# Performance work log

Hardware: AMD Instinct MI355X
Metric: run time of the kernel (lower is better)

Reference implementation:

```python
import jax, jax.numpy as jnp
import numpy as np

INPUT_SIZE = 16
HIDDEN = 256


def setup_inputs() -> dict:
    key = jax.random.key(0)
    ks = jax.random.split(key, 12)
    B, T, F, H = 512, 168, INPUT_SIZE, HIDDEN
    s_ih = 1.0 / np.sqrt(H)
    def u(k, shape):
        return jax.random.uniform(k, shape, jnp.float32, -s_ih, s_ih)
    return {
        "x": jax.random.normal(ks[0], (B, T, F), jnp.float32),
        # LSTM params, torch gate order (i, f, g, o) stacked along dim 0
        "w_ih": u(ks[1], (4 * H, F)),
        "w_hh": u(ks[2], (4 * H, H)),
        "b_ih": u(ks[3], (4 * H,)),
        "b_hh": u(ks[4], (4 * H,)),
        # MLP params
        "fc1_w": u(ks[5], (128, H)),
        "fc1_b": u(ks[6], (128,)),
        "fc2_w": u(ks[7], (64, 128)),
        "fc2_b": u(ks[8], (64,)),
        "fc3_w": u(ks[9], (1, 64)),
        "fc3_b": u(ks[10], (1,)),
    }


def _lstm(x, w_ih, w_hh, b_ih, b_hh):
    B, T, F = x.shape
    H = w_hh.shape[1]
    # Precompute input contribution for all timesteps: [B, T, 4H]
    x_proj = jnp.einsum("btf,gf->btg", x, w_ih) + b_ih + b_hh

    def step(carry, xp_t):
        h, c = carry
        gates = xp_t + h @ w_hh.T  # [B, 4H]
        i, f, g, o = jnp.split(gates, 4, axis=-1)
        i = jax.nn.sigmoid(i)
        f = jax.nn.sigmoid(f)
        g = jnp.tanh(g)
        o = jax.nn.sigmoid(o)
        c = f * c + i * g
        h = o * jnp.tanh(c)
        return (h, c), h

    h0 = jnp.zeros((B, H), x.dtype)
    c0 = jnp.zeros((B, H), x.dtype)
    (_, _), hs = jax.lax.scan(step, (h0, c0), jnp.swapaxes(x_proj, 0, 1))
    return jnp.swapaxes(hs, 0, 1)  # [B, T, H]


def reference(x, w_ih, w_hh, b_ih, b_hh, fc1_w, fc1_b, fc2_w, fc2_b, fc3_w, fc3_b):
    h = _lstm(x, w_ih, w_hh, b_ih, b_hh)          # [B, T, H]
    h = jax.nn.relu(h @ fc1_w.T + fc1_b)           # [B, T, 128]
    h = jax.nn.relu(h @ fc2_w.T + fc2_b)           # [B, T, 64]
    out = h @ fc3_w.T + fc3_b                      # [B, T, 1]
    return out
```

## Files before the change

### kernel.cpp

```cpp
#include <hip/hip_runtime.h>

typedef _Float16 half8 __attribute__((ext_vector_type(8)));
typedef float floatx4 __attribute__((ext_vector_type(4)));
typedef unsigned uint4v __attribute__((ext_vector_type(4)));

#define Bsz 512
#define Tsz 168
#define Fsz 16
#define Hsz 256
#define KTILES 9
#define LDS_K 296

#define WSW_OFF   0
#define BIAS_OFF  589824
#define FC1_OFF   593920
#define FC2_OFF   659456
#define HH_OFF    675840
#define XBUF_OFF  (HH_OFF + 44040192)

__global__ __launch_bounds__(256) void k_prep(
    const float* __restrict__ w_hh, const float* __restrict__ w_ih,
    const float* __restrict__ b_ih, const float* __restrict__ b_hh,
    const float* __restrict__ fc1_w, const float* __restrict__ fc2_w,
    _Float16* __restrict__ wsw, float* __restrict__ bias,
    _Float16* __restrict__ w1f, _Float16* __restrict__ w2f) {
    const int b = blockIdx.x, tid = threadIdx.x;
    const int lane = tid & 63, sub = tid >> 6;
    if (b < 144) {
        int tile = b * 4 + sub;
        int nt = tile / KTILES, kt = tile - nt * KTILES;
        int n_in = lane & 15, kg = lane >> 4;
        int J = nt >> 2, g = nt & 3;
        int n_orig = g * 256 + J * 16 + n_in;
        half8 v;
#pragma unroll
        for (int e = 0; e < 8; ++e) {
            int k = kt * 32 + kg * 8 + e;
            float f;
            if (k < 256)      f = w_hh[n_orig * 256 + k];
            else if (k < 272) f = w_ih[n_orig * 16 + (k - 256)];
            else              f = 0.0f;
            v[e] = (_Float16)f;
        }
        ((half8*)wsw)[tile * 64 + lane] = v;
    } else if (b < 148) {
        int id = (b - 144) * 256 + tid;
        int nt = id >> 4, n = id & 15;
        int J = nt >> 2, g = nt & 3;
        int n_orig = g * 256 + J * 16 + n;
        bias[id] = b_ih[n_orig] + b_hh[n_orig];
    } else if (b < 164) {
        int tile = (b - 148) * 4 + sub;
        int nt = tile >> 3, kt = tile & 7;
        int n_in = lane & 15, kg = lane >> 4;
        half8 v;
#pragma unroll
        for (int e = 0; e < 8; ++e)
            v[e] = (_Float16)fc1_w[(nt * 16 + n_in) * 256 + kt * 32 + kg * 8 + e];
        ((half8*)w1f)[tile * 64 + lane] = v;
    } else {
        int tile = (b - 164) * 4 + sub;
        int nt = tile >> 2, kt = tile & 3;
        int n_in = lane & 15, kg = lane >> 4;
        half8 v;
#pragma unroll
        for (int e = 0; e < 8; ++e)
            v[e] = (_Float16)fc2_w[(nt * 16 + n_in) * 128 + kt * 32 + kg * 8 + e];
        ((half8*)w2f)[tile * 64 + lane] = v;
    }
}

__global__ __launch_bounds__(512, 1) void k_lstm14(
    const float* __restrict__ x, const _Float16* __restrict__ wsw,
    const float* __restrict__ bias, unsigned* __restrict__ hh32,
    unsigned long long* __restrict__ xbuf) {
    __shared__ __align__(16) _Float16 h_lds[16][LDS_K];
    __shared__ float glds[4][16][68];

    const int tid = threadIdx.x;
    const int wave = tid >> 6, lane = tid & 63;
    const int n_in = lane & 15, quad = lane >> 4;
    const int bb = blockIdx.x & 31, ng = blockIdx.x >> 5;
    const int b0 = bb * 16;
    const int Jl = wave & 3;
    const int gp = wave >> 2;

    float bs[2];
    half8 wf[2][KTILES];
#pragma unroll
    for (int gg = 0; gg < 2; ++gg) {
        const int nt = ng * 16 + Jl * 4 + gp * 2 + gg;
        bs[gg] = bias[nt * 16 + n_in];
#pragma unroll
        for (int kt = 0; kt < KTILES; ++kt)
            wf[gg][kt] = ((const half8*)wsw)[((size_t)nt * KTILES + kt) * 64 + lane];
    }

    for (int i = tid; i < 16 * LDS_K; i += 512)
        ((_Float16*)h_lds)[i] = (_Float16)0.0f;
    __syncthreads();
    if (tid < 256) {
        int m = tid >> 4, f = tid & 15;
        h_lds[m][Hsz + f] = (_Float16)x[((b0 + m) * Tsz + 0) * Fsz + f];
    }
    __syncthreads();

    const int cm = tid >> 5, cj = tid & 31;
    float c_st[2] = {0.f, 0.f};

    for (int t = 0; t < Tsz; ++t) {
        half8 afr[KTILES];
#pragma unroll
        for (int kt = 0; kt < KTILES; ++kt)
            afr[kt] = *(const half8*)&h_lds[n_in][kt * 32 + quad * 8];

        floatx4 acc[2] = {(floatx4){0.f,0.f,0.f,0.f}, (floatx4){0.f,0.f,0.f,0.f}};
#pragma unroll
        for (int gg = 0; gg < 2; ++gg) {
#pragma unroll
            for (int kt = 0; kt < KTILES; ++kt)
                acc[gg] = __builtin_amdgcn_mfma_f32_16x16x32_f16(afr[kt], wf[gg][kt], acc[gg], 0, 0, 0);
        }

#pragma unroll
        for (int gg = 0; gg < 2; ++gg)
#pragma unroll
            for (int r = 0; r < 4; ++r)
                glds[gp * 2 + gg][quad * 4 + r][Jl * 16 + n_in] = acc[gg][r] + bs[gg];
        __syncthreads();

        union { _Float16 f[2]; unsigned u; } pk;
#pragma unroll
        for (int e = 0; e < 2; ++e) {
            int jl = 2 * cj + e;
            float ig = glds[0][cm][jl];
            float fg = glds[1][cm][jl];
            float gg_ = glds[2][cm][jl];
            float og = glds[3][cm][jl];
            float si = 1.0f / (1.0f + __expf(-ig));
            float sf = 1.0f / (1.0f + __expf(-fg));
            float tg = 1.0f - 2.0f / (__expf(2.0f * gg_) + 1.0f);
            float so = 1.0f / (1.0f + __expf(-og));
            float c = sf * c_st[e] + si * tg;
            c_st[e] = c;
            float th = 1.0f - 2.0f / (__expf(2.0f * c) + 1.0f);
            pk.f[e] = (_Float16)(so * th);
        }
        *(unsigned*)&h_lds[cm][ng * 64 + 2 * cj] = pk.u;

        const size_t rb = ((size_t)((bb * 2 + (t & 1)) * 16));
        if (t + 1 < Tsz) {
            unsigned long long pv = ((unsigned long long)pk.u << 32) | (unsigned)(t + 1);
            __hip_atomic_store(&xbuf[(rb + cm) * 128 + ng * 32 + cj], pv,
                               __ATOMIC_RELAXED, __HIP_MEMORY_SCOPE_AGENT);
        }
        __builtin_nontemporal_store(
            pk.u, &hh32[((size_t)(b0 + cm) * Tsz + t) * 128 + ng * 32 + cj]);

        if (t + 1 < Tsz) {
            float xr = 0.0f;
            if (tid < 256)
                xr = x[((b0 + (tid >> 4)) * Tsz + (t + 1)) * Fsz + (tid & 15)];

            const unsigned want = (unsigned)(t + 1);
            unsigned long long* p1 = &xbuf[(rb + cm) * 128 + ((ng + 1) & 3) * 32 + cj];
            unsigned long long* p2 = &xbuf[(rb + cm) * 128 + ((ng + 2) & 3) * 32 + cj];
            unsigned long long* p3 = &xbuf[(rb + cm) * 128 + ((ng + 3) & 3) * 32 + cj];
            unsigned long long v1 = __hip_atomic_load(p1, __ATOMIC_RELAXED,
                                                      __HIP_MEMORY_SCOPE_AGENT);
            unsigned long long v2 = __hip_atomic_load(p2, __ATOMIC_RELAXED,
                                                      __HIP_MEMORY_SCOPE_AGENT);
            unsigned long long v3 = __hip_atomic_load(p3, __ATOMIC_RELAXED,
                                                      __HIP_MEMORY_SCOPE_AGENT);
            while ((unsigned)v1 != want || (unsigned)v2 != want || (unsigned)v3 != want) {
                if ((unsigned)v1 != want)
                    v1 = __hip_atomic_load(p1, __ATOMIC_RELAXED, __HIP_MEMORY_SCOPE_AGENT);
                if ((unsigned)v2 != want)
                    v2 = __hip_atomic_load(p2, __ATOMIC_RELAXED, __HIP_MEMORY_SCOPE_AGENT);
                if ((unsigned)v3 != want)
                    v3 = __hip_atomic_load(p3, __ATOMIC_RELAXED, __HIP_MEMORY_SCOPE_AGENT);
            }
            *(unsigned*)&h_lds[cm][((ng + 1) & 3) * 64 + 2 * cj] = (unsigned)(v1 >> 32);
            *(unsigned*)&h_lds[cm][((ng + 2) & 3) * 64 + 2 * cj] = (unsigned)(v2 >> 32);
            *(unsigned*)&h_lds[cm][((ng + 3) & 3) * 64 + 2 * cj] = (unsigned)(v3 >> 32);
            if (tid < 256)
                h_lds[tid >> 4][Hsz + (tid & 15)] = (_Float16)xr;
            __syncthreads();
        }
    }
}

__global__ __launch_bounds__(512, 1) void k_mlp5(
    const _Float16* __restrict__ hh, const _Float16* __restrict__ w1f,
    const _Float16* __restrict__ w2f, const float* __restrict__ b1,
    const float* __restrict__ b2, const float* __restrict__ w3,
    const float* __restrict__ b3, float* __restrict__ out) {
    __shared__ __align__(16) _Float16 w1sh[64 * 512];
    __shared__ __align__(16) _Float16 w2sh[16 * 512];
    __shared__ _Float16 st1[8][16][136];
    __shared__ _Float16 st2[8][16][72];

    const int tid = threadIdx.x;
    const int wave = tid >> 6, lane = tid & 63;
    const int n_in = lane & 15, quad = lane >> 4;
    const int nchunks = (Bsz * Tsz) / 128;

    {
        float4* d1 = (float4*)w1sh;
        const float4* s1 = (const float4*)w1f;
#pragma unroll
        for (int it = 0; it < 8; ++it) d1[it * 512 + tid] = s1[it * 512 + tid];
        float4* d2 = (float4*)w2sh;
        const float4* s2 = (const float4*)w2f;
#pragma unroll
        for (int it = 0; it < 2; ++it) d2[it * 512 + tid] = s2[it * 512 + tid];
    }
    __syncthreads();

    uint4v rawA[8], rawB[8];
    if (blockIdx.x < nchunks) {
        const int tok0 = blockIdx.x * 128 + wave * 16;
#pragma unroll
        for (int kt = 0; kt < 8; ++kt)
            rawA[kt] = __builtin_nontemporal_load(
                (const uint4v*)&hh[(size_t)(tok0 + n_in) * 256 + kt * 32 + quad * 8]);
    }

    for (int chunk = blockIdx.x; chunk < nchunks; chunk += gridDim.x) {
        const int nxt = chunk + gridDim.x;
        if (nxt < nchunks) {
            const int tok0n = nxt * 128 + wave * 16;
#pragma unroll
            for (int kt = 0; kt < 8; ++kt)
                rawB[kt] = __builtin_nontemporal_load(
                    (const uint4v*)&hh[(size_t)(tok0n + n_in) * 256 + kt * 32 + quad * 8]);
        }

        const int tok0 = chunk * 128 + wave * 16;
        half8 afr[8];
#pragma unroll
        for (int kt = 0; kt < 8; ++kt)
            afr[kt] = __builtin_bit_cast(half8, rawA[kt]);

#pragma unroll
        for (int nt = 0; nt < 8; ++nt) {
            floatx4 a = (floatx4){0.f, 0.f, 0.f, 0.f};
#pragma unroll
            for (int kt = 0; kt < 8; ++kt) {
                half8 bfr = *(const half8*)&w1sh[(nt * 8 + kt) * 512 + lane * 8];
                a = __builtin_amdgcn_mfma_f32_16x16x32_f16(afr[kt], bfr, a, 0, 0, 0);
            }
            float bb = b1[nt * 16 + n_in];
#pragma unroll
            for (int r = 0; r < 4; ++r) {
                float v = a[r] + bb;
                st1[wave][quad * 4 + r][nt * 16 + n_in] = (_Float16)(v > 0.f ? v : 0.f);
            }
        }

        half8 a2[4];
#pragma unroll
        for (int kt = 0; kt < 4; ++kt)
            a2[kt] = *(const half8*)&st1[wave][n_in][kt * 32 + quad * 8];
#pragma unroll
        for (int nt = 0; nt < 4; ++nt) {
            floatx4 a = (floatx4){0.f, 0.f, 0.f, 0.f};
#pragma unroll
            for (int kt = 0; kt < 4; ++kt) {
                half8 bfr = *(const half8*)&w2sh[(nt * 4 + kt) * 512 + lane * 8];
                a = __builtin_amdgcn_mfma_f32_16x16x32_f16(a2[kt], bfr, a, 0, 0, 0);
            }
            float bb = b2[nt * 16 + n_in];
#pragma unroll
            for (int r = 0; r < 4; ++r) {
                float v = a[r] + bb;
                st2[wave][quad * 4 + r][nt * 16 + n_in] = (_Float16)(v > 0.f ? v : 0.f);
            }
        }

        float p = 0.0f;
#pragma unroll
        for (int e = 0; e < 16; ++e)
            p += (float)st2[wave][n_in][quad * 16 + e] * w3[quad * 16 + e];
        p += __shfl_down(p, 32);
        p += __shfl_down(p, 16);
        if (quad == 0) out[tok0 + n_in] = p + b3[0];

#pragma unroll
        for (int kt = 0; kt < 8; ++kt) rawA[kt] = rawB[kt];
    }
}

extern "C" void kernel_launch(void* const* d_in, const int* in_sizes, int n_in,
                              void* d_out, int out_size, void* d_ws, size_t ws_size,
                              hipStream_t stream) {
    const float* x     = (const float*)d_in[0];
    const float* w_ih  = (const float*)d_in[1];
    const float* w_hh  = (const float*)d_in[2];
    const float* b_ih  = (const float*)d_in[3];
    const float* b_hh  = (const float*)d_in[4];
    const float* fc1_w = (const float*)d_in[5];
    const float* fc1_b = (const float*)d_in[6];
    const float* fc2_w = (const float*)d_in[7];
    const float* fc2_b = (const float*)d_in[8];
    const float* fc3_w = (const float*)d_in[9];
    const float* fc3_b = (const float*)d_in[10];

    char* ws = (char*)d_ws;
    _Float16* wsw  = (_Float16*)(ws + WSW_OFF);
    float*    bias = (float*)(ws + BIAS_OFF);
    _Float16* w1f  = (_Float16*)(ws + FC1_OFF);
    _Float16* w2f  = (_Float16*)(ws + FC2_OFF);
    _Float16* hhist= (_Float16*)(ws + HH_OFF);
    unsigned long long* xbuf = (unsigned long long*)(ws + XBUF_OFF);

    k_prep<<<168, 256, 0, stream>>>(w_hh, w_ih, b_ih, b_hh, fc1_w, fc2_w,
                                    wsw, bias, w1f, w2f);
    k_lstm14<<<128, 512, 0, stream>>>(x, wsw, bias, (unsigned*)hhist, xbuf);
    k_mlp5<<<224, 512, 0, stream>>>(hhist, w1f, w2f, fc1_b, fc2_b,
                                    fc3_w, fc3_b, (float*)d_out);
}
```

Measured before the change: 423.3 us.

## Drop prep kernel, convert weights in-kernel, fixed 3-chunk MLP prefetch

Removes the separate weight-prep kernel; the LSTM and MLP kernels now read fp32 weights and convert them to fp16 fragments themselves, which saves one launch and a workspace round trip. The x load for the next step is moved to the start of each timestep, the local h store is moved after the atomic publish, and the spin loop reloads all three flags unconditionally. The MLP kernel replaces its strided double-buffered loop with three chunk loads issued up front and then computed, which assumes exactly 672 chunks across 224 blocks. Launch bounds change to allow 2 blocks per CU, which may raise register pressure.

```diff
diff --git a/kernel.cpp b/kernel.cpp
--- a/kernel.cpp
+++ b/kernel.cpp
@@ -11,68 +11,13 @@
 #define KTILES 9
 #define LDS_K 296
 
-#define WSW_OFF   0
-#define BIAS_OFF  589824
-#define FC1_OFF   593920
-#define FC2_OFF   659456
 #define HH_OFF    675840
 #define XBUF_OFF  (HH_OFF + 44040192)
 
-__global__ __launch_bounds__(256) void k_prep(
-    const float* __restrict__ w_hh, const float* __restrict__ w_ih,
-    const float* __restrict__ b_ih, const float* __restrict__ b_hh,
-    const float* __restrict__ fc1_w, const float* __restrict__ fc2_w,
-    _Float16* __restrict__ wsw, float* __restrict__ bias,
-    _Float16* __restrict__ w1f, _Float16* __restrict__ w2f) {
-    const int b = blockIdx.x, tid = threadIdx.x;
-    const int lane = tid & 63, sub = tid >> 6;
-    if (b < 144) {
-        int tile = b * 4 + sub;
-        int nt = tile / KTILES, kt = tile - nt * KTILES;
-        int n_in = lane & 15, kg = lane >> 4;
-        int J = nt >> 2, g = nt & 3;
-        int n_orig = g * 256 + J * 16 + n_in;
-        half8 v;
-#pragma unroll
-        for (int e = 0; e < 8; ++e) {
-            int k = kt * 32 + kg * 8 + e;
-            float f;
-            if (k < 256)      f = w_hh[n_orig * 256 + k];
-            else if (k < 272) f = w_ih[n_orig * 16 + (k - 256)];
-            else              f = 0.0f;
-            v[e] = (_Float16)f;
-        }
-        ((half8*)wsw)[tile * 64 + lane] = v;
-    } else if (b < 148) {
-        int id = (b - 144) * 256 + tid;
-        int nt = id >> 4, n = id & 15;
-        int J = nt >> 2, g = nt & 3;
-        int n_orig = g * 256 + J * 16 + n;
-        bias[id] = b_ih[n_orig] + b_hh[n_orig];
-    } else if (b < 164) {
-        int tile = (b - 148) * 4 + sub;
-        int nt = tile >> 3, kt = tile & 7;
-        int n_in = lane & 15, kg = lane >> 4;
-        half8 v;
-#pragma unroll
-        for (int e = 0; e < 8; ++e)
-            v[e] = (_Float16)fc1_w[(nt * 16 + n_in) * 256 + kt * 32 + kg * 8 + e];
-        ((half8*)w1f)[tile * 64 + lane] = v;
-    } else {
-        int tile = (b - 164) * 4 + sub;
-        int nt = tile >> 2, kt = tile & 3;
-        int n_in = lane & 15, kg = lane >> 4;
-        half8 v;
-#pragma unroll
-        for (int e = 0; e < 8; ++e)
-            v[e] = (_Float16)fc2_w[(nt * 16 + n_in) * 128 + kt * 32 + kg * 8 + e];
-        ((half8*)w2f)[tile * 64 + lane] = v;
-    }
-}
-
-__global__ __launch_bounds__(512, 1) void k_lstm14(
-    const float* __restrict__ x, const _Float16* __restrict__ wsw,
-    const float* __restrict__ bias, unsigned* __restrict__ hh32,
+__global__ __launch_bounds__(512, 2) void k_lstm15(
+    const float* __restrict__ x, const float* __restrict__ w_ih,
+    const float* __restrict__ w_hh, const float* __restrict__ b_ih,
+    const float* __restrict__ b_hh, unsigned* __restrict__ hh32,
     unsigned long long* __restrict__ xbuf) {
     __shared__ __align__(16) _Float16 h_lds[16][LDS_K];
     __shared__ float glds[4][16][68];
@@ -84,16 +29,34 @@
     const int b0 = bb * 16;
     const int Jl = wave & 3;
     const int gp = wave >> 2;
+    (void)wave;
 
     float bs[2];
     half8 wf[2][KTILES];
 #pragma unroll
     for (int gg = 0; gg < 2; ++gg) {
         const int nt = ng * 16 + Jl * 4 + gp * 2 + gg;
-        bs[gg] = bias[nt * 16 + n_in];
-#pragma unroll
-        for (int kt = 0; kt < KTILES; ++kt)
-            wf[gg][kt] = ((const half8*)wsw)[((size_t)nt * KTILES + kt) * 64 + lane];
+        const int J = nt >> 2, g = nt & 3;
+        const int n_orig = g * 256 + J * 16 + n_in;
+        bs[gg] = b_ih[n_orig] + b_hh[n_orig];
+#pragma unroll
+        for (int kt = 0; kt < 8; ++kt) {
+            const float* src = &w_hh[n_orig * 256 + kt * 32 + quad * 8];
+            half8 v;
+#pragma unroll
+            for (int e = 0; e < 8; ++e) v[e] = (_Float16)src[e];
+            wf[gg][kt] = v;
+        }
+        half8 vx;
+        if (quad < 2) {
+            const float* srcx = &w_ih[n_orig * 16 + quad * 8];
+#pragma unroll
+            for (int e = 0; e < 8; ++e) vx[e] = (_Float16)srcx[e];
+        } else {
+#pragma unroll
+            for (int e = 0; e < 8; ++e) vx[e] = (_Float16)0.0f;
+        }
+        wf[gg][8] = vx;
     }
 
     for (int i = tid; i < 16 * LDS_K; i += 512)
@@ -109,6 +72,10 @@
     float c_st[2] = {0.f, 0.f};
 
     for (int t = 0; t < Tsz; ++t) {
+        float xr = 0.0f;
+        if (t + 1 < Tsz && tid < 256)
+            xr = x[((b0 + (tid >> 4)) * Tsz + (t + 1)) * Fsz + (tid & 15)];
+
         half8 afr[KTILES];
 #pragma unroll
         for (int kt = 0; kt < KTILES; ++kt)
@@ -146,7 +113,6 @@
             float th = 1.0f - 2.0f / (__expf(2.0f * c) + 1.0f);
             pk.f[e] = (_Float16)(so * th);
         }
-        *(unsigned*)&h_lds[cm][ng * 64 + 2 * cj] = pk.u;
 
         const size_t rb = ((size_t)((bb * 2 + (t & 1)) * 16));
         if (t + 1 < Tsz) {
@@ -154,14 +120,11 @@
             __hip_atomic_store(&xbuf[(rb + cm) * 128 + ng * 32 + cj], pv,
                                __ATOMIC_RELAXED, __HIP_MEMORY_SCOPE_AGENT);
         }
+        *(unsigned*)&h_lds[cm][ng * 64 + 2 * cj] = pk.u;
         __builtin_nontemporal_store(
             pk.u, &hh32[((size_t)(b0 + cm) * Tsz + t) * 128 + ng * 32 + cj]);
 
         if (t + 1 < Tsz) {
-            float xr = 0.0f;
-            if (tid < 256)
-                xr = x[((b0 + (tid >> 4)) * Tsz + (t + 1)) * Fsz + (tid & 15)];
-
             const unsigned want = (unsigned)(t + 1);
             unsigned long long* p1 = &xbuf[(rb + cm) * 128 + ((ng + 1) & 3) * 32 + cj];
             unsigned long long* p2 = &xbuf[(rb + cm) * 128 + ((ng + 2) & 3) * 32 + cj];
@@ -173,12 +136,9 @@
             unsigned long long v3 = __hip_atomic_load(p3, __ATOMIC_RELAXED,
                                                       __HIP_MEMORY_SCOPE_AGENT);
             while ((unsigned)v1 != want || (unsigned)v2 != want || (unsigned)v3 != want) {
-                if ((unsigned)v1 != want)
-                    v1 = __hip_atomic_load(p1, __ATOMIC_RELAXED, __HIP_MEMORY_SCOPE_AGENT);
-                if ((unsigned)v2 != want)
-                    v2 = __hip_atomic_load(p2, __ATOMIC_RELAXED, __HIP_MEMORY_SCOPE_AGENT);
-                if ((unsigned)v3 != want)
-                    v3 = __hip_atomic_load(p3, __ATOMIC_RELAXED, __HIP_MEMORY_SCOPE_AGENT);
+                v1 = __hip_atomic_load(p1, __ATOMIC_RELAXED, __HIP_MEMORY_SCOPE_AGENT);
+                v2 = __hip_atomic_load(p2, __ATOMIC_RELAXED, __HIP_MEMORY_SCOPE_AGENT);
+                v3 = __hip_atomic_load(p3, __ATOMIC_RELAXED, __HIP_MEMORY_SCOPE_AGENT);
             }
             *(unsigned*)&h_lds[cm][((ng + 1) & 3) * 64 + 2 * cj] = (unsigned)(v1 >> 32);
             *(unsigned*)&h_lds[cm][((ng + 2) & 3) * 64 + 2 * cj] = (unsigned)(v2 >> 32);
@@ -190,9 +150,9 @@
     }
 }
 
-__global__ __launch_bounds__(512, 1) void k_mlp5(
-    const _Float16* __restrict__ hh, const _Float16* __restrict__ w1f,
-    const _Float16* __restrict__ w2f, const float* __restrict__ b1,
+__global__ __launch_bounds__(512, 2) void k_mlp6(
+    const _Float16* __restrict__ hh, const float* __restrict__ fc1_w,
+    const float* __restrict__ fc2_w, const float* __restrict__ b1,
     const float* __restrict__ b2, const float* __restrict__ w3,
     const float* __restrict__ b3, float* __restrict__ out) {
     __shared__ __align__(16) _Float16 w1sh[64 * 512];
@@ -203,44 +163,56 @@
     const int tid = threadIdx.x;
     const int wave = tid >> 6, lane = tid & 63;
     const int n_in = lane & 15, quad = lane >> 4;
-    const int nchunks = (Bsz * Tsz) / 128;
 
     {
-        float4* d1 = (float4*)w1sh;
-        const float4* s1 = (const float4*)w1f;
-#pragma unroll
-        for (int it = 0; it < 8; ++it) d1[it * 512 + tid] = s1[it * 512 + tid];
-        float4* d2 = (float4*)w2sh;
-        const float4* s2 = (const float4*)w2f;
-#pragma unroll
-        for (int it = 0; it < 2; ++it) d2[it * 512 + tid] = s2[it * 512 + tid];
+#pragma unroll
+        for (int it = 0; it < 8; ++it) {
+            int s = it * 512 + tid;
+            int tile = s >> 6, ln = s & 63;
+            int nt = tile >> 3, kt = tile & 7, ni = ln & 15, kg = ln >> 4;
+            const float* src = &fc1_w[(nt * 16 + ni) * 256 + kt * 32 + kg * 8];
+            half8 v;
+#pragma unroll
+            for (int e = 0; e < 8; ++e) v[e] = (_Float16)src[e];
+            ((half8*)w1sh)[s] = v;
+        }
+#pragma unroll
+        for (int it = 0; it < 2; ++it) {
+            int s = it * 512 + tid;
+            int tile = s >> 6, ln = s & 63;
+            int nt = tile >> 2, kt = tile & 3, ni = ln & 15, kg = ln >> 4;
+            const float* src = &fc2_w[(nt * 16 + ni) * 128 + kt * 32 + kg * 8];
+            half8 v;
+#pragma unroll
+            for (int e = 0; e < 8; ++e) v[e] = (_Float16)src[e];
+            ((half8*)w2sh)[s] = v;
+        }
     }
     __syncthreads();
 
-    uint4v rawA[8], rawB[8];
-    if (blockIdx.x < nchunks) {
-        const int tok0 = blockIdx.x * 128 + wave * 16;
-#pragma unroll
-        for (int kt = 0; kt < 8; ++kt)
-            rawA[kt] = __builtin_nontemporal_load(
-                (const uint4v*)&hh[(size_t)(tok0 + n_in) * 256 + kt * 32 + quad * 8]);
-    }
-
-    for (int chunk = blockIdx.x; chunk < nchunks; chunk += gridDim.x) {
-        const int nxt = chunk + gridDim.x;
-        if (nxt < nchunks) {
-            const int tok0n = nxt * 128 + wave * 16;
-#pragma unroll
-            for (int kt = 0; kt < 8; ++kt)
-                rawB[kt] = __builtin_nontemporal_load(
-                    (const uint4v*)&hh[(size_t)(tok0n + n_in) * 256 + kt * 32 + quad * 8]);
-        }
-
+    uint4v bufA[8], bufB[8], bufC[8];
+    const int ch0 = blockIdx.x, ch1 = blockIdx.x + 224, ch2 = blockIdx.x + 448;
+
+#define MLP_LOAD(dst, ch)                                                      \
+    {                                                                          \
+        const int tok0_ = (ch) * 128 + wave * 16;                              \
+        _Pragma("unroll")                                                      \
+        for (int kt = 0; kt < 8; ++kt)                                         \
+            dst[kt] = __builtin_nontemporal_load(                              \
+                (const uint4v*)&hh[(size_t)(tok0_ + n_in) * 256 + kt * 32 +    \
+                                   quad * 8]);                                 \
+    }
+
+    MLP_LOAD(bufA, ch0)
+    MLP_LOAD(bufB, ch1)
+    MLP_LOAD(bufC, ch2)
+
+    auto compute = [&](const uint4v* raw, int chunk) {
         const int tok0 = chunk * 128 + wave * 16;
         half8 afr[8];
 #pragma unroll
         for (int kt = 0; kt < 8; ++kt)
-            afr[kt] = __builtin_bit_cast(half8, rawA[kt]);
+            afr[kt] = __builtin_bit_cast(half8, raw[kt]);
 
 #pragma unroll
         for (int nt = 0; nt < 8; ++nt) {
@@ -250,10 +222,10 @@
                 half8 bfr = *(const half8*)&w1sh[(nt * 8 + kt) * 512 + lane * 8];
                 a = __builtin_amdgcn_mfma_f32_16x16x32_f16(afr[kt], bfr, a, 0, 0, 0);
             }
-            float bb = b1[nt * 16 + n_in];
+            float bbv = b1[nt * 16 + n_in];
 #pragma unroll
             for (int r = 0; r < 4; ++r) {
-                float v = a[r] + bb;
+                float v = a[r] + bbv;
                 st1[wave][quad * 4 + r][nt * 16 + n_in] = (_Float16)(v > 0.f ? v : 0.f);
             }
         }
@@ -270,10 +242,10 @@
                 half8 bfr = *(const half8*)&w2sh[(nt * 4 + kt) * 512 + lane * 8];
                 a = __builtin_amdgcn_mfma_f32_16x16x32_f16(a2[kt], bfr, a, 0, 0, 0);
             }
-            float bb = b2[nt * 16 + n_in];
+            float bbv = b2[nt * 16 + n_in];
 #pragma unroll
             for (int r = 0; r < 4; ++r) {
-                float v = a[r] + bb;
+                float v = a[r] + bbv;
                 st2[wave][quad * 4 + r][nt * 16 + n_in] = (_Float16)(v > 0.f ? v : 0.f);
             }
         }
@@ -285,10 +257,12 @@
         p += __shfl_down(p, 32);
         p += __shfl_down(p, 16);
         if (quad == 0) out[tok0 + n_in] = p + b3[0];
-
-#pragma unroll
-        for (int kt = 0; kt < 8; ++kt) rawA[kt] = rawB[kt];
-    }
+    };
+
+    compute(bufA, ch0);
+    compute(bufB, ch1);
+    compute(bufC, ch2);
+#undef MLP_LOAD
 }
 
 extern "C" void kernel_launch(void* const* d_in, const int* in_sizes, int n_in,
@@ -307,16 +281,11 @@
     const float* fc3_b = (const float*)d_in[10];
 
     char* ws = (char*)d_ws;
-    _Float16* wsw  = (_Float16*)(ws + WSW_OFF);
-    float*    bias = (float*)(ws + BIAS_OFF);
-    _Float16* w1f  = (_Float16*)(ws + FC1_OFF);
-    _Float16* w2f  = (_Float16*)(ws + FC2_OFF);
     _Float16* hhist= (_Float16*)(ws + HH_OFF);
     unsigned long long* xbuf = (unsigned long long*)(ws + XBUF_OFF);
 
-    k_prep<<<168, 256, 0, stream>>>(w_hh, w_ih, b_ih, b_hh, fc1_w, fc2_w,
-                                    wsw, bias, w1f, w2f);
-    k_lstm14<<<128, 512, 0, stream>>>(x, wsw, bias, (unsigned*)hhist, xbuf);
-    k_mlp5<<<224, 512, 0, stream>>>(hhist, w1f, w2f, fc1_b, fc2_b,
+    k_lstm15<<<128, 512, 0, stream>>>(x, w_ih, w_hh, b_ih, b_hh,
+                                      (unsigned*)hhist, xbuf);
+    k_mlp6<<<224, 512, 0, stream>>>(hhist, fc1_w, fc2_w, fc1_b, fc2_b,
                                     fc3_w, fc3_b, (float*)d_out);
 }
```

Result: slower. 492.5 us (+16.3%).
